# Kernel tuning notes

Hardware: AMD Instinct MI355X
Metric: run time of the kernel (lower is better)

The kernel has to match this reference:

```python
import jax, jax.numpy as jnp
import numpy as np

N = 100000   # total nodes (batched graphs)
E = 800000   # random edges (self-loops appended -> E+N total)
G = 2000     # number of graphs in batch
H = 4        # heads per GAT layer
D = 64       # hidden_size (per-head out dim)
IN = 64      # in_feats
EXTRA = 8    # extra graph-level feats
HID = H * D  # 256


def setup_inputs() -> dict:
    key = jax.random.key(0)
    ks = jax.random.split(key, 24)
    s = 0.5  # init std used in the torch module
    feats_node = jax.random.normal(ks[0], (N, IN), jnp.float32)
    feats_graph = jax.random.normal(ks[1], (G, EXTRA), jnp.float32)
    # edges + self loops (DGL GATConv requires no zero-in-degree nodes)
    src = jnp.concatenate([jax.random.randint(ks[2], (E,), 0, N), jnp.arange(N)])
    dst = jnp.concatenate([jax.random.randint(ks[3], (E,), 0, N), jnp.arange(N)])
    node_gid = jnp.sort(jax.random.randint(ks[4], (N,), 0, G))
    # GAT layer 1
    W1 = jax.random.normal(ks[5], (IN, HID), jnp.float32) * s
    al1 = jax.random.normal(ks[6], (H, D), jnp.float32) * s
    ar1 = jax.random.normal(ks[7], (H, D), jnp.float32) * s
    b1 = jnp.zeros((HID,), jnp.float32)
    # GAT layer 2
    W2 = jax.random.normal(ks[8], (HID, HID), jnp.float32) * s
    al2 = jax.random.normal(ks[9], (H, D), jnp.float32) * s
    ar2 = jax.random.normal(ks[10], (H, D), jnp.float32) * s
    b2 = jnp.zeros((HID,), jnp.float32)
    # WeightedAverage readout score
    Ws = jax.random.normal(ks[11], (HID, 1), jnp.float32) * s
    bs = jnp.zeros((1,), jnp.float32)
    # MLP: 264 -> 128 -> 64 -> 1 with SELU
    Wm1 = jax.random.normal(ks[12], (HID + EXTRA, 2 * D), jnp.float32) * s
    bm1 = jnp.zeros((2 * D,), jnp.float32)
    Wm2 = jax.random.normal(ks[13], (2 * D, D), jnp.float32) * s
    bm2 = jnp.zeros((D,), jnp.float32)
    Wm3 = jax.random.normal(ks[14], (D, 1), jnp.float32) * s
    bm3 = jnp.zeros((1,), jnp.float32)
    return dict(feats_node=feats_node, feats_graph=feats_graph,
                W1=W1, al1=al1, ar1=ar1, b1=b1,
                W2=W2, al2=al2, ar2=ar2, b2=b2,
                Ws=Ws, bs=bs, Wm1=Wm1, bm1=bm1, Wm2=Wm2, bm2=bm2,
                Wm3=Wm3, bm3=bm3,
                src=src, dst=dst, node_gid=node_gid)


def gat_layer(x, W, al, ar, b, src, dst):
    # DGL GATConv: fc -> per-node attn projections -> edge leaky_relu ->
    # edge softmax over incoming edges -> weighted scatter-sum -> +bias
    f = (x @ W).reshape(N, H, D)                       # [N,H,D]
    el = jnp.einsum('nhd,hd->nh', f, al)               # [N,H]
    er = jnp.einsum('nhd,hd->nh', f, ar)               # [N,H]
    e = jax.nn.leaky_relu(el[src] + er[dst], 0.2)      # [E',H]
    m = jax.ops.segment_max(e, dst, num_segments=N)    # per-dst max
    e = jnp.exp(e - m[dst])
    denom = jax.ops.segment_sum(e, dst, num_segments=N)
    alpha = e / denom[dst]                             # edge softmax [E',H]
    out = jax.ops.segment_sum(alpha[:, :, None] * f[src], dst, num_segments=N)
    return out.reshape(N, HID) + b


def reference(feats_node, feats_graph, W1, al1, ar1, b1, W2, al2, ar2, b2,
              Ws, bs, Wm1, bm1, Wm2, bm2, Wm3, bm3, src, dst, node_gid):
    x = jax.nn.relu(gat_layer(feats_node, W1, al1, ar1, b1, src, dst))
    x = jax.nn.relu(gat_layer(x, W2, al2, ar2, b2, src, dst))
    # weighted-average readout per graph: sum(w*x)/sum(w)
    w = jax.nn.sigmoid(x @ Ws + bs)                    # [N,1]
    num = jax.ops.segment_sum(w * x, node_gid, num_segments=G)
    den = jax.ops.segment_sum(w, node_gid, num_segments=G)
    emb = num / jnp.where(den == 0, 1.0, den)          # [G,HID]
    h = jnp.concatenate([emb, feats_graph], axis=1)    # [G,HID+EXTRA]
    h = jax.nn.selu(h @ Wm1 + bm1)
    h = jax.nn.selu(h @ Wm2 + bm2)
    return h @ Wm3 + bm3                               # [G,1]
```

## Files before the change

### kernel.cpp

```cpp
#include <hip/hip_runtime.h>
#include <hip/hip_bf16.h>
#include <math.h>

#define NN     100000
#define GG     2000
#define HH     4
#define DD     64
#define HID    256
#define INF_   64
#define EXTRA  8

typedef unsigned short u16;
typedef __attribute__((ext_vector_type(8))) short bf16x8;
typedef __attribute__((ext_vector_type(4))) float f32x4;

__device__ __forceinline__ u16 f2bf(float f) {
    unsigned u = __float_as_uint(f);
    return (u16)((u + 0x7fffu + ((u >> 16) & 1u)) >> 16);
}
__device__ __forceinline__ float bf2f(u16 v) {
    return __uint_as_float(((unsigned)v) << 16);
}

__global__ __launch_bounds__(256) void wsplit_kernel(
    const float* __restrict__ W, u16* __restrict__ hi, u16* __restrict__ lo,
    int K, int lgK)
{
    int idx = blockIdx.x * 256 + threadIdx.x;
    if (idx >= 256 * K) return;
    int n = idx >> lgK, k = idx & (K - 1);
    float w = W[k * HID + n];
    u16 h = f2bf(w);
    hi[idx] = h;
    lo[idx] = f2bf(w - bf2f(h));
}

__global__ __launch_bounds__(256) void walprep_kernel(
    const float* __restrict__ W1, const float* __restrict__ al,
    const float* __restrict__ ar, float* __restrict__ wal, float* __restrict__ war)
{
    int tid = threadIdx.x;
    int d = tid >> 2, h = tid & 3;
    const float* wrow = W1 + d * HID + h * DD;
    const float* av = al + h * DD;
    const float* bv = ar + h * DD;
    float s1 = 0.f, s2 = 0.f;
    for (int c = 0; c < DD; ++c) { s1 += wrow[c] * av[c]; s2 += wrow[c] * bv[c]; }
    wal[d * 4 + h] = s1;
    war[d * 4 + h] = s2;
}

__global__ __launch_bounds__(256) void elr1_kernel(
    const float* __restrict__ feats, const float* __restrict__ wal,
    const float* __restrict__ war, float* __restrict__ el, float* __restrict__ er)
{
    int idx = blockIdx.x * 256 + threadIdx.x;
    if (idx >= NN * HH) return;
    int n = idx >> 2, h = idx & 3;
    const float* f = feats + (size_t)n * INF_;
    float s1 = 0.f, s2 = 0.f;
    #pragma unroll 4
    for (int d = 0; d < INF_; d += 4) {
        float4 fv = *reinterpret_cast<const float4*>(f + d);
        s1 += fv.x * wal[(d + 0) * 4 + h] + fv.y * wal[(d + 1) * 4 + h]
            + fv.z * wal[(d + 2) * 4 + h] + fv.w * wal[(d + 3) * 4 + h];
        s2 += fv.x * war[(d + 0) * 4 + h] + fv.y * war[(d + 1) * 4 + h]
            + fv.z * war[(d + 2) * 4 + h] + fv.w * war[(d + 3) * 4 + h];
    }
    el[idx] = s1;
    er[idx] = s2;
}

__global__ __launch_bounds__(256) void aggregate_feats_kernel(
    const float* __restrict__ feats, const float* __restrict__ w,
    const float* __restrict__ invden, const int* __restrict__ rowptr,
    const int* __restrict__ colsrc, float* __restrict__ Y1)
{
    int t = blockIdx.x * 4 + (threadIdx.x >> 6);
    int lane = threadIdx.x & 63;
    if (t >= NN) return;
    int beg = rowptr[t], end = rowptr[t + 1];
    float a0 = 0.f, a1 = 0.f, a2 = 0.f, a3 = 0.f;
    float b0 = 0.f, b1 = 0.f, b2 = 0.f, b3 = 0.f;
    int i = beg;
    for (; i + 1 < end; i += 2) {
        int s0 = colsrc[i], s1 = colsrc[i + 1];
        float4 w0 = *reinterpret_cast<const float4*>(w + (size_t)i * 4);
        float4 w1 = *reinterpret_cast<const float4*>(w + (size_t)(i + 1) * 4);
        float f0 = feats[(size_t)s0 * INF_ + lane];
        float f1 = feats[(size_t)s1 * INF_ + lane];
        a0 += w0.x * f0; a1 += w0.y * f0; a2 += w0.z * f0; a3 += w0.w * f0;
        b0 += w1.x * f1; b1 += w1.y * f1; b2 += w1.z * f1; b3 += w1.w * f1;
    }
    if (i < end) {
        int s0 = colsrc[i];
        float4 w0 = *reinterpret_cast<const float4*>(w + (size_t)i * 4);
        float f0 = feats[(size_t)s0 * INF_ + lane];
        a0 += w0.x * f0; a1 += w0.y * f0; a2 += w0.z * f0; a3 += w0.w * f0;
    }
    float4 inv = *reinterpret_cast<const float4*>(invden + (size_t)t * 4);
    float* y = Y1 + (size_t)t * HID;
    y[lane]       = (a0 + b0) * inv.x;
    y[64 + lane]  = (a1 + b1) * inv.y;
    y[128 + lane] = (a2 + b2) * inv.z;
    y[192 + lane] = (a3 + b3) * inv.w;
}

__global__ __launch_bounds__(256) void gemm_head_kernel(
    const float* __restrict__ Y1, const u16* __restrict__ BThi,
    const u16* __restrict__ BTlo, const float* __restrict__ bias,
    float* __restrict__ X1, int M)
{
    const int tid  = threadIdx.x;
    const int wv   = tid >> 6, lane = tid & 63;
    const int quad = lane >> 4, l15 = lane & 15;
    const int r0 = blockIdx.x * 128;
    const int cbase = wv * 64;

    f32x4 acc[8][4];
    #pragma unroll
    for (int i = 0; i < 8; ++i)
        #pragma unroll
        for (int j = 0; j < 4; ++j)
            acc[i][j] = (f32x4){0.f, 0.f, 0.f, 0.f};

    #pragma unroll
    for (int k0 = 0; k0 < 64; k0 += 32) {
        bf16x8 bh[4], bl[4];
        #pragma unroll
        for (int j = 0; j < 4; ++j) {
            int n = cbase + j * 16 + l15;
            bh[j] = *reinterpret_cast<const bf16x8*>(BThi + (size_t)n * 64 + k0 + quad * 8);
            bl[j] = *reinterpret_cast<const bf16x8*>(BTlo + (size_t)n * 64 + k0 + quad * 8);
        }
        #pragma unroll
        for (int i = 0; i < 8; ++i) {
            int gr = min(r0 + i * 16 + l15, M - 1);
            const float* ap = Y1 + (size_t)gr * HID + cbase + k0 + quad * 8;
            float4 va0 = *reinterpret_cast<const float4*>(ap);
            float4 va1 = *reinterpret_cast<const float4*>(ap + 4);
            float av[8] = {va0.x, va0.y, va0.z, va0.w, va1.x, va1.y, va1.z, va1.w};
            bf16x8 vh, vl;
            #pragma unroll
            for (int m = 0; m < 8; ++m) {
                u16 h = f2bf(av[m]);
                vh[m] = (short)h;
                vl[m] = (short)f2bf(av[m] - bf2f(h));
            }
            #pragma unroll
            for (int j = 0; j < 4; ++j) {
                acc[i][j] = __builtin_amdgcn_mfma_f32_16x16x32_bf16(vh, bh[j], acc[i][j], 0, 0, 0);
                acc[i][j] = __builtin_amdgcn_mfma_f32_16x16x32_bf16(vl, bh[j], acc[i][j], 0, 0, 0);
                acc[i][j] = __builtin_amdgcn_mfma_f32_16x16x32_bf16(vh, bl[j], acc[i][j], 0, 0, 0);
            }
        }
    }
    float bv[4];
    #pragma unroll
    for (int j = 0; j < 4; ++j) bv[j] = bias[cbase + j * 16 + l15];
    #pragma unroll
    for (int i = 0; i < 8; ++i)
        #pragma unroll
        for (int rr = 0; rr < 4; ++rr) {
            int grow = r0 + i * 16 + quad * 4 + rr;
            if (grow < M) {
                float* xrow = X1 + (size_t)grow * HID + cbase + l15;
                #pragma unroll
                for (int j = 0; j < 4; ++j)
                    xrow[j * 16] = fmaxf(acc[i][j][rr] + bv[j], 0.f);
            }
        }
}

template<bool BF16_OUT>
__global__ __launch_bounds__(256) void mfma_gemm_kernel(
    const float* __restrict__ A, const u16* __restrict__ BThi,
    const u16* __restrict__ BTlo, float* __restrict__ Cf, u16* __restrict__ Cb,
    const float* __restrict__ al, const float* __restrict__ ar,
    float* __restrict__ el, float* __restrict__ er, int M, int K)
{
    __shared__ __align__(16) u16 Ah[128 * 40];
    __shared__ __align__(16) u16 Al[128 * 40];
    __shared__ __align__(16) u16 Bh[128 * 40];
    __shared__ __align__(16) u16 Bl[128 * 40];
    const int tid  = threadIdx.x;
    const int wave = tid >> 6, lane = tid & 63;
    const int quad = lane >> 4, l15 = lane & 15;
    const int wy = wave >> 1, wx = wave & 1;
    const int r0 = blockIdx.x * 128, c0 = blockIdx.y * 128;
    const int sr = tid >> 2, sseg = tid & 3;

    f32x4 acc[4][4];
    #pragma unroll
    for (int i = 0; i < 4; ++i)
        #pragma unroll
        for (int j = 0; j < 4; ++j)
            acc[i][j] = (f32x4){0.f, 0.f, 0.f, 0.f};

    for (int k0 = 0; k0 < K; k0 += 32) {
        #pragma unroll
        for (int half = 0; half < 2; ++half) {
            int r = sr + half * 64;
            int gr = min(r0 + r, M - 1);
            const float* ap = A + (size_t)gr * K + k0 + sseg * 8;
            float4 va0 = *reinterpret_cast<const float4*>(ap);
            float4 va1 = *reinterpret_cast<const float4*>(ap + 4);
            float av[8] = {va0.x, va0.y, va0.z, va0.w, va1.x, va1.y, va1.z, va1.w};
            bf16x8 vh, vl;
            #pragma unroll
            for (int m = 0; m < 8; ++m) {
                u16 h = f2bf(av[m]);
                vh[m] = (short)h;
                vl[m] = (short)f2bf(av[m] - bf2f(h));
            }
            *reinterpret_cast<bf16x8*>(&Ah[r * 40 + sseg * 8]) = vh;
            *reinterpret_cast<bf16x8*>(&Al[r * 40 + sseg * 8]) = vl;
            int gc = c0 + r;
            *reinterpret_cast<bf16x8*>(&Bh[r * 40 + sseg * 8]) =
                *reinterpret_cast<const bf16x8*>(BThi + (size_t)gc * K + k0 + sseg * 8);
            *reinterpret_cast<bf16x8*>(&Bl[r * 40 + sseg * 8]) =
                *reinterpret_cast<const bf16x8*>(BTlo + (size_t)gc * K + k0 + sseg * 8);
        }
        __syncthreads();
        bf16x8 afh[4], afl[4], bfh[4], bfl[4];
        #pragma unroll
        for (int i = 0; i < 4; ++i) {
            int row = (wy * 64 + i * 16 + l15) * 40 + quad * 8;
            afh[i] = *reinterpret_cast<const bf16x8*>(&Ah[row]);
            afl[i] = *reinterpret_cast<const bf16x8*>(&Al[row]);
        }
        #pragma unroll
        for (int j = 0; j < 4; ++j) {
            int row = (wx * 64 + j * 16 + l15) * 40 + quad * 8;
            bfh[j] = *reinterpret_cast<const bf16x8*>(&Bh[row]);
            bfl[j] = *reinterpret_cast<const bf16x8*>(&Bl[row]);
        }
        #pragma unroll
        for (int i = 0; i < 4; ++i)
            #pragma unroll
            for (int j = 0; j < 4; ++j) {
                acc[i][j] = __builtin_amdgcn_mfma_f32_16x16x32_bf16(afh[i], bfh[j], acc[i][j], 0, 0, 0);
                acc[i][j] = __builtin_amdgcn_mfma_f32_16x16x32_bf16(afl[i], bfh[j], acc[i][j], 0, 0, 0);
                acc[i][j] = __builtin_amdgcn_mfma_f32_16x16x32_bf16(afh[i], bfl[j], acc[i][j], 0, 0, 0);
            }
        __syncthreads();
    }

    #pragma unroll
    for (int i = 0; i < 4; ++i)
        #pragma unroll
        for (int rr = 0; rr < 4; ++rr) {
            int grow = r0 + wy * 64 + i * 16 + quad * 4 + rr;
            if (grow < M) {
                if (BF16_OUT) {
                    u16* crow = Cb + (size_t)grow * HID + c0 + wx * 64 + l15;
                    #pragma unroll
                    for (int j = 0; j < 4; ++j) crow[j * 16] = f2bf(acc[i][j][rr]);
                } else {
                    float* crow = Cf + (size_t)grow * HID + c0 + wx * 64 + l15;
                    #pragma unroll
                    for (int j = 0; j < 4; ++j) crow[j * 16] = acc[i][j][rr];
                }
            }
        }

    const int h = blockIdx.y * 2 + wx;
    float alf[4], arf[4];
    #pragma unroll
    for (int j = 0; j < 4; ++j) {
        alf[j] = al[h * DD + j * 16 + l15];
        arf[j] = ar[h * DD + j * 16 + l15];
    }
    #pragma unroll
    for (int i = 0; i < 4; ++i)
        #pragma unroll
        for (int rr = 0; rr < 4; ++rr) {
            float sl = acc[i][0][rr] * alf[0] + acc[i][1][rr] * alf[1]
                     + acc[i][2][rr] * alf[2] + acc[i][3][rr] * alf[3];
            float sr_ = acc[i][0][rr] * arf[0] + acc[i][1][rr] * arf[1]
                      + acc[i][2][rr] * arf[2] + acc[i][3][rr] * arf[3];
            #pragma unroll
            for (int off = 1; off < 16; off <<= 1) {
                sl  += __shfl_xor(sl, off, 64);
                sr_ += __shfl_xor(sr_, off, 64);
            }
            if (l15 == 0) {
                int grow = r0 + wy * 64 + i * 16 + quad * 4 + rr;
                if (grow < M) {
                    el[grow * 4 + h] = sl;
                    er[grow * 4 + h] = sr_;
                }
            }
        }
}

__device__ __forceinline__ float leaky02(float x) { return x > 0.f ? x : 0.2f * x; }

__global__ __launch_bounds__(256) void edge_softmax_kernel(
    const float* __restrict__ el, const float* __restrict__ er,
    const int* __restrict__ rowptr, const int* __restrict__ colsrc,
    float* __restrict__ w, float* __restrict__ invden)
{
    int idx = blockIdx.x * 256 + threadIdx.x;
    if (idx >= NN * HH) return;
    int t = idx >> 2, h = idx & 3;
    int beg = rowptr[t], end = rowptr[t + 1];
    float ert = er[idx];
    float m = -1e30f;
    for (int i = beg; i < end; ++i) {
        int s = colsrc[i];
        m = fmaxf(m, leaky02(el[s * 4 + h] + ert));
    }
    float den = 0.f;
    for (int i = beg; i < end; ++i) {
        int s = colsrc[i];
        float v = expf(leaky02(el[s * 4 + h] + ert) - m);
        w[(size_t)i * 4 + h] = v;
        den += v;
    }
    invden[idx] = 1.f / den;
}

__global__ __launch_bounds__(256) void aggregate_bf16_kernel(
    const u16* __restrict__ F, const float* __restrict__ w,
    const float* __restrict__ invden, const int* __restrict__ rowptr,
    const int* __restrict__ colsrc, const float* __restrict__ bias,
    u16* __restrict__ out)
{
    int t = blockIdx.x * 4 + (threadIdx.x >> 6);
    int lane = threadIdx.x & 63;
    if (t >= NN) return;
    int beg = rowptr[t], end = rowptr[t + 1];
    const int h = lane >> 4;
    float4 acc0 = make_float4(0.f, 0.f, 0.f, 0.f);
    float4 acc1 = make_float4(0.f, 0.f, 0.f, 0.f);
    int i = beg;
    for (; i + 1 < end; i += 2) {
        int s0 = colsrc[i], s1 = colsrc[i + 1];
        float w0 = w[(size_t)i * 4 + h];
        float w1 = w[(size_t)(i + 1) * 4 + h];
        ushort4 f0 = *reinterpret_cast<const ushort4*>(F + (size_t)s0 * HID + 4 * lane);
        ushort4 f1 = *reinterpret_cast<const ushort4*>(F + (size_t)s1 * HID + 4 * lane);
        acc0.x += w0 * bf2f(f0.x); acc0.y += w0 * bf2f(f0.y);
        acc0.z += w0 * bf2f(f0.z); acc0.w += w0 * bf2f(f0.w);
        acc1.x += w1 * bf2f(f1.x); acc1.y += w1 * bf2f(f1.y);
        acc1.z += w1 * bf2f(f1.z); acc1.w += w1 * bf2f(f1.w);
    }
    if (i < end) {
        int s0 = colsrc[i];
        float w0 = w[(size_t)i * 4 + h];
        ushort4 f0 = *reinterpret_cast<const ushort4*>(F + (size_t)s0 * HID + 4 * lane);
        acc0.x += w0 * bf2f(f0.x); acc0.y += w0 * bf2f(f0.y);
        acc0.z += w0 * bf2f(f0.z); acc0.w += w0 * bf2f(f0.w);
    }
    float inv = invden[t * 4 + h];
    float4 bv = *reinterpret_cast<const float4*>(bias + 4 * lane);
    ushort4 r;
    r.x = f2bf(fmaxf((acc0.x + acc1.x) * inv + bv.x, 0.f));
    r.y = f2bf(fmaxf((acc0.y + acc1.y) * inv + bv.y, 0.f));
    r.z = f2bf(fmaxf((acc0.z + acc1.z) * inv + bv.z, 0.f));
    r.w = f2bf(fmaxf((acc0.w + acc1.w) * inv + bv.w, 0.f));
    *reinterpret_cast<ushort4*>(out + (size_t)t * HID + 4 * lane) = r;
}

__global__ __launch_bounds__(256) void readout_kernel(
    const u16* __restrict__ X, const float* __restrict__ Ws,
    const float* __restrict__ bs, const int* __restrict__ gptr,
    float* __restrict__ emb)
{
    int g = blockIdx.x * 4 + (threadIdx.x >> 6);
    int lane = threadIdx.x & 63;
    if (g >= GG) return;
    int beg = gptr[g], end = gptr[g + 1];
    float4 wv = *reinterpret_cast<const float4*>(Ws + 4 * lane);
    float b = bs[0];
    float4 acc = make_float4(0.f, 0.f, 0.f, 0.f);
    float wsum = 0.f;
    for (int n = beg; n < end; ++n) {
        ushort4 xv = *reinterpret_cast<const ushort4*>(X + (size_t)n * HID + 4 * lane);
        float x0 = bf2f(xv.x), x1 = bf2f(xv.y), x2 = bf2f(xv.z), x3 = bf2f(xv.w);
        float p = x0 * wv.x + x1 * wv.y + x2 * wv.z + x3 * wv.w;
        #pragma unroll
        for (int off = 32; off; off >>= 1) p += __shfl_xor(p, off, 64);
        float w = 1.f / (1.f + expf(-(p + b)));
        wsum += w;
        acc.x += w * x0; acc.y += w * x1; acc.z += w * x2; acc.w += w * x3;
    }
    float inv = (wsum == 0.f) ? 1.f : wsum;
    float4 e;
    e.x = acc.x / inv; e.y = acc.y / inv; e.z = acc.z / inv; e.w = acc.w / inv;
    *reinterpret_cast<float4*>(emb + (size_t)g * HID + 4 * lane) = e;
}

__device__ __forceinline__ float selu_f(float x)
{
    const float scale = 1.0507009873554805f, alpha = 1.6732632423543772f;
    return scale * (x > 0.f ? x : alpha * expm1f(x));
}

__global__ __launch_bounds__(128) void mlp_kernel(
    const float* __restrict__ emb, const float* __restrict__ fg,
    const float* __restrict__ Wm1, const float* __restrict__ bm1,
    const float* __restrict__ Wm2, const float* __restrict__ bm2,
    const float* __restrict__ Wm3, const float* __restrict__ bm3,
    float* __restrict__ out)
{
    int g = blockIdx.x;
    __shared__ float h[HID + EXTRA];
    __shared__ float h1[128];
    __shared__ float h2[64];
    int tid = threadIdx.x;
    h[tid] = emb[(size_t)g * HID + tid];
    h[128 + tid] = emb[(size_t)g * HID + 128 + tid];
    if (tid < EXTRA) h[HID + tid] = fg[(size_t)g * EXTRA + tid];
    __syncthreads();
    float acc = bm1[tid];
    for (int i = 0; i < HID + EXTRA; ++i) acc += h[i] * Wm1[i * 128 + tid];
    h1[tid] = selu_f(acc);
    __syncthreads();
    if (tid < 64) {
        float acc2 = bm2[tid];
        for (int i = 0; i < 128; ++i) acc2 += h1[i] * Wm2[i * 64 + tid];
        h2[tid] = selu_f(acc2);
    }
    __syncthreads();
    if (tid < 64) {
        float p = h2[tid] * Wm3[tid];
        #pragma unroll
        for (int off = 32; off; off >>= 1) p += __shfl_xor(p, off, 64);
        if (tid == 0) out[g] = p + bm3[0];
    }
}

__global__ void count_dst_kernel(const int* __restrict__ dst, int* __restrict__ cnt, int E)
{
    int e = blockIdx.x * 256 + threadIdx.x;
    if (e < E) atomicAdd(&cnt[dst[e]], 1);
}
__global__ void count_gid_kernel(const int* __restrict__ gid, int* __restrict__ cnt, int n)
{
    int i = blockIdx.x * 256 + threadIdx.x;
    if (i < n) atomicAdd(&cnt[gid[i]], 1);
}
__global__ void fill_csr_kernel(const int* __restrict__ src, const int* __restrict__ dst,
                                int* __restrict__ cursor, int* __restrict__ colsrc, int E)
{
    int e = blockIdx.x * 256 + threadIdx.x;
    if (e < E) {
        int p = atomicAdd(&cursor[dst[e]], 1);
        colsrc[p] = src[e];
    }
}

__global__ __launch_bounds__(256) void scan_blocks_kernel(
    const int* __restrict__ in, int n, int* __restrict__ out, int* __restrict__ partials)
{
    __shared__ int lds[256];
    int tid = threadIdx.x;
    int base = blockIdx.x * 1024 + tid * 4;
    int v0 = (base + 0 < n) ? in[base + 0] : 0;
    int v1 = (base + 1 < n) ? in[base + 1] : 0;
    int v2 = (base + 2 < n) ? in[base + 2] : 0;
    int v3 = (base + 3 < n) ? in[base + 3] : 0;
    int s = v0 + v1 + v2 + v3;
    lds[tid] = s;
    __syncthreads();
    for (int off = 1; off < 256; off <<= 1) {
        int t = (tid >= off) ? lds[tid - off] : 0;
        __syncthreads();
        lds[tid] += t;
        __syncthreads();
    }
    int excl = lds[tid] - s;
    if (base + 0 < n) out[base + 0] = excl;
    if (base + 1 < n) out[base + 1] = excl + v0;
    if (base + 2 < n) out[base + 2] = excl + v0 + v1;
    if (base + 3 < n) out[base + 3] = excl + v0 + v1 + v2;
    if (tid == 255) partials[blockIdx.x] = lds[255];
}

__global__ __launch_bounds__(256) void scan_partials_kernel(int* partials, int nb)
{
    __shared__ int lds[256];
    int tid = threadIdx.x;
    int v = (tid < nb) ? partials[tid] : 0;
    lds[tid] = v;
    __syncthreads();
    for (int off = 1; off < 256; off <<= 1) {
        int t = (tid >= off) ? lds[tid - off] : 0;
        __syncthreads();
        lds[tid] += t;
        __syncthreads();
    }
    int excl = lds[tid] - v;
    if (tid < nb) partials[tid] = excl;
}

__global__ void add_offsets_kernel(int* __restrict__ out, const int* __restrict__ partials, int n)
{
    int i = blockIdx.x * 256 + threadIdx.x;
    if (i < n) out[i] += partials[i >> 10];
}

extern "C" void kernel_launch(void* const* d_in, const int* in_sizes, int n_in,
                              void* d_out, int out_size, void* d_ws, size_t ws_size,
                              hipStream_t stream)
{
    const float* feats_node  = (const float*)d_in[0];
    const float* feats_graph = (const float*)d_in[1];
    const float* W1  = (const float*)d_in[2];
    const float* al1 = (const float*)d_in[3];
    const float* ar1 = (const float*)d_in[4];
    const float* b1  = (const float*)d_in[5];
    const float* W2  = (const float*)d_in[6];
    const float* al2 = (const float*)d_in[7];
    const float* ar2 = (const float*)d_in[8];
    const float* b2  = (const float*)d_in[9];
    const float* Ws  = (const float*)d_in[10];
    const float* bs  = (const float*)d_in[11];
    const float* Wm1 = (const float*)d_in[12];
    const float* bm1 = (const float*)d_in[13];
    const float* Wm2 = (const float*)d_in[14];
    const float* bm2 = (const float*)d_in[15];
    const float* Wm3 = (const float*)d_in[16];
    const float* bm3 = (const float*)d_in[17];
    const int* src = (const int*)d_in[18];
    const int* dst = (const int*)d_in[19];
    const int* gid = (const int*)d_in[20];
    float* out = (float*)d_out;
    const int E = in_sizes[18];

    char* p = (char*)d_ws;
    auto alloc = [&](size_t bytes) {
        char* r = p;
        p += (bytes + 255) & ~(size_t)255;
        return r;
    };
    float* Y1     = (float*)alloc((size_t)NN * HID * 4);
    float* X      = (float*)alloc((size_t)NN * HID * 4);
    float* el     = (float*)alloc((size_t)NN * HH * 4);
    float* er     = (float*)alloc((size_t)NN * HH * 4);
    float* wbuf   = (float*)alloc((size_t)E * HH * 4);
    float* invden = (float*)alloc((size_t)NN * HH * 4);
    int*   cnt    = (int*)alloc((size_t)(NN + 1) * 4);
    int*   rowptr = (int*)alloc((size_t)(NN + 1) * 4);
    int*   colsrc = (int*)alloc((size_t)E * 4);
    int*   gcnt   = (int*)alloc((size_t)(GG + 1) * 4);
    int*   gptr   = (int*)alloc((size_t)(GG + 1) * 4);
    int*   parts  = (int*)alloc(1024 * 4);
    float* emb    = (float*)alloc((size_t)GG * HID * 4);
    u16*   BT1h   = (u16*)alloc((size_t)HID * INF_ * 2);
    u16*   BT1l   = (u16*)alloc((size_t)HID * INF_ * 2);
    u16*   BT2h   = (u16*)alloc((size_t)HID * HID * 2);
    u16*   BT2l   = (u16*)alloc((size_t)HID * HID * 2);
    float* wal1   = (float*)alloc(INF_ * HH * 4);
    float* war1   = (float*)alloc(INF_ * HH * 4);
    u16*   Fbf2   = (u16*)Y1;
    u16*   Xbf2   = (u16*)X;

    hipMemsetAsync(cnt, 0, (size_t)(NN + 1) * 4, stream);
    count_dst_kernel<<<(E + 255) / 256, 256, 0, stream>>>(dst, cnt, E);
    {
        int n = NN + 1, nb = (n + 1023) / 1024;
        scan_blocks_kernel<<<nb, 256, 0, stream>>>(cnt, n, rowptr, parts);
        scan_partials_kernel<<<1, 256, 0, stream>>>(parts, nb);
        add_offsets_kernel<<<(n + 255) / 256, 256, 0, stream>>>(rowptr, parts, n);
    }
    hipMemcpyAsync(cnt, rowptr, (size_t)(NN + 1) * 4, hipMemcpyDeviceToDevice, stream);
    fill_csr_kernel<<<(E + 255) / 256, 256, 0, stream>>>(src, dst, cnt, colsrc, E);

    hipMemsetAsync(gcnt, 0, (size_t)(GG + 1) * 4, stream);
    count_gid_kernel<<<(NN + 255) / 256, 256, 0, stream>>>(gid, gcnt, NN);
    {
        int n = GG + 1, nb = (n + 1023) / 1024;
        scan_blocks_kernel<<<nb, 256, 0, stream>>>(gcnt, n, gptr, parts);
        scan_partials_kernel<<<1, 256, 0, stream>>>(parts, nb);
        add_offsets_kernel<<<(n + 255) / 256, 256, 0, stream>>>(gptr, parts, n);
    }

    wsplit_kernel<<<(HID * INF_ + 255) / 256, 256, 0, stream>>>(W1, BT1h, BT1l, INF_, 6);
    wsplit_kernel<<<(HID * HID + 255) / 256, 256, 0, stream>>>(W2, BT2h, BT2l, HID, 8);
    walprep_kernel<<<1, 256, 0, stream>>>(W1, al1, ar1, wal1, war1);

    const int nh_blocks = (NN * HH + 255) / 256;

    elr1_kernel<<<nh_blocks, 256, 0, stream>>>(feats_node, wal1, war1, el, er);
    edge_softmax_kernel<<<nh_blocks, 256, 0, stream>>>(el, er, rowptr, colsrc, wbuf, invden);
    aggregate_feats_kernel<<<(NN + 3) / 4, 256, 0, stream>>>(feats_node, wbuf, invden,
                                                             rowptr, colsrc, Y1);
    gemm_head_kernel<<<(NN + 127) / 128, 256, 0, stream>>>(Y1, BT1h, BT1l, b1, X, NN);

    dim3 ggrid((NN + 127) / 128, HID / 128);
    mfma_gemm_kernel<true><<<ggrid, 256, 0, stream>>>(
        X, BT2h, BT2l, nullptr, Fbf2, al2, ar2, el, er, NN, HID);
    edge_softmax_kernel<<<nh_blocks, 256, 0, stream>>>(el, er, rowptr, colsrc, wbuf, invden);
    aggregate_bf16_kernel<<<(NN + 3) / 4, 256, 0, stream>>>(Fbf2, wbuf, invden, rowptr, colsrc,
                                                            b2, Xbf2);

    readout_kernel<<<(GG + 3) / 4, 256, 0, stream>>>(Xbf2, Ws, bs, gptr, emb);
    mlp_kernel<<<GG, 128, 0, stream>>>(emb, feats_graph, Wm1, bm1, Wm2, bm2, Wm3, bm3, out);
}
```

Before: 645.4 us.

## Load GEMM fragments directly from global memory and cache edge logits in softmax

The MFMA GEMM kernel no longer stages A and B tiles through shared memory with two block barriers per k-step. Each wave now loads its own A rows (splitting them into bf16 hi/lo parts) and its B fragments straight from global memory into registers. Separately, the edge softmax first pass stores the leaky-relu logits into w, so the second pass reads them back instead of re-gathering el through colsrc. The GEMM change removes LDS traffic and barriers, but the A split is now computed twice per block across the wx waves and B is read without shared reuse, which may raise global/L2 traffic.

```diff
diff --git a/kernel.cpp b/kernel.cpp
--- a/kernel.cpp
+++ b/kernel.cpp
@@ -179,16 +179,12 @@
     const float* __restrict__ al, const float* __restrict__ ar,
     float* __restrict__ el, float* __restrict__ er, int M, int K)
 {
-    __shared__ __align__(16) u16 Ah[128 * 40];
-    __shared__ __align__(16) u16 Al[128 * 40];
-    __shared__ __align__(16) u16 Bh[128 * 40];
-    __shared__ __align__(16) u16 Bl[128 * 40];
     const int tid  = threadIdx.x;
     const int wave = tid >> 6, lane = tid & 63;
     const int quad = lane >> 4, l15 = lane & 15;
     const int wy = wave >> 1, wx = wave & 1;
-    const int r0 = blockIdx.x * 128, c0 = blockIdx.y * 128;
-    const int sr = tid >> 2, sseg = tid & 3;
+    const int r0 = blockIdx.x * 128 + wy * 64;
+    const int c0 = blockIdx.y * 128 + wx * 64;
 
     f32x4 acc[4][4];
     #pragma unroll
@@ -198,11 +194,17 @@
             acc[i][j] = (f32x4){0.f, 0.f, 0.f, 0.f};
 
     for (int k0 = 0; k0 < K; k0 += 32) {
-        #pragma unroll
-        for (int half = 0; half < 2; ++half) {
-            int r = sr + half * 64;
-            int gr = min(r0 + r, M - 1);
-            const float* ap = A + (size_t)gr * K + k0 + sseg * 8;
+        bf16x8 bh[4], bl[4];
+        #pragma unroll
+        for (int j = 0; j < 4; ++j) {
+            size_t boff = (size_t)(c0 + j * 16 + l15) * K + k0 + quad * 8;
+            bh[j] = *reinterpret_cast<const bf16x8*>(BThi + boff);
+            bl[j] = *reinterpret_cast<const bf16x8*>(BTlo + boff);
+        }
+        #pragma unroll
+        for (int i = 0; i < 4; ++i) {
+            int gr = min(r0 + i * 16 + l15, M - 1);
+            const float* ap = A + (size_t)gr * K + k0 + quad * 8;
             float4 va0 = *reinterpret_cast<const float4*>(ap);
             float4 va1 = *reinterpret_cast<const float4*>(ap + 4);
             float av[8] = {va0.x, va0.y, va0.z, va0.w, va1.x, va1.y, va1.z, va1.w};
@@ -213,51 +215,27 @@
                 vh[m] = (short)h;
                 vl[m] = (short)f2bf(av[m] - bf2f(h));
             }
-            *reinterpret_cast<bf16x8*>(&Ah[r * 40 + sseg * 8]) = vh;
-            *reinterpret_cast<bf16x8*>(&Al[r * 40 + sseg * 8]) = vl;
-            int gc = c0 + r;
-            *reinterpret_cast<bf16x8*>(&Bh[r * 40 + sseg * 8]) =
-                *reinterpret_cast<const bf16x8*>(BThi + (size_t)gc * K + k0 + sseg * 8);
-            *reinterpret_cast<bf16x8*>(&Bl[r * 40 + sseg * 8]) =
-                *reinterpret_cast<const bf16x8*>(BTlo + (size_t)gc * K + k0 + sseg * 8);
-        }
-        __syncthreads();
-        bf16x8 afh[4], afl[4], bfh[4], bfl[4];
-        #pragma unroll
-        for (int i = 0; i < 4; ++i) {
-            int row = (wy * 64 + i * 16 + l15) * 40 + quad * 8;
-            afh[i] = *reinterpret_cast<const bf16x8*>(&Ah[row]);
-            afl[i] = *reinterpret_cast<const bf16x8*>(&Al[row]);
-        }
-        #pragma unroll
-        for (int j = 0; j < 4; ++j) {
-            int row = (wx * 64 + j * 16 + l15) * 40 + quad * 8;
-            bfh[j] = *reinterpret_cast<const bf16x8*>(&Bh[row]);
-            bfl[j] = *reinterpret_cast<const bf16x8*>(&Bl[row]);
-        }
-        #pragma unroll
-        for (int i = 0; i < 4; ++i)
             #pragma unroll
             for (int j = 0; j < 4; ++j) {
-                acc[i][j] = __builtin_amdgcn_mfma_f32_16x16x32_bf16(afh[i], bfh[j], acc[i][j], 0, 0, 0);
-                acc[i][j] = __builtin_amdgcn_mfma_f32_16x16x32_bf16(afl[i], bfh[j], acc[i][j], 0, 0, 0);
-                acc[i][j] = __builtin_amdgcn_mfma_f32_16x16x32_bf16(afh[i], bfl[j], acc[i][j], 0, 0, 0);
-            }
-        __syncthreads();
+                acc[i][j] = __builtin_amdgcn_mfma_f32_16x16x32_bf16(vh, bh[j], acc[i][j], 0, 0, 0);
+                acc[i][j] = __builtin_amdgcn_mfma_f32_16x16x32_bf16(vl, bh[j], acc[i][j], 0, 0, 0);
+                acc[i][j] = __builtin_amdgcn_mfma_f32_16x16x32_bf16(vh, bl[j], acc[i][j], 0, 0, 0);
+            }
+        }
     }
 
     #pragma unroll
     for (int i = 0; i < 4; ++i)
         #pragma unroll
         for (int rr = 0; rr < 4; ++rr) {
-            int grow = r0 + wy * 64 + i * 16 + quad * 4 + rr;
+            int grow = r0 + i * 16 + quad * 4 + rr;
             if (grow < M) {
                 if (BF16_OUT) {
-                    u16* crow = Cb + (size_t)grow * HID + c0 + wx * 64 + l15;
+                    u16* crow = Cb + (size_t)grow * HID + c0 + l15;
                     #pragma unroll
                     for (int j = 0; j < 4; ++j) crow[j * 16] = f2bf(acc[i][j][rr]);
                 } else {
-                    float* crow = Cf + (size_t)grow * HID + c0 + wx * 64 + l15;
+                    float* crow = Cf + (size_t)grow * HID + c0 + l15;
                     #pragma unroll
                     for (int j = 0; j < 4; ++j) crow[j * 16] = acc[i][j][rr];
                 }
@@ -285,7 +263,7 @@
                 sr_ += __shfl_xor(sr_, off, 64);
             }
             if (l15 == 0) {
-                int grow = r0 + wy * 64 + i * 16 + quad * 4 + rr;
+                int grow = r0 + i * 16 + quad * 4 + rr;
                 if (grow < M) {
                     el[grow * 4 + h] = sl;
                     er[grow * 4 + h] = sr_;
@@ -309,12 +287,13 @@
     float m = -1e30f;
     for (int i = beg; i < end; ++i) {
         int s = colsrc[i];
-        m = fmaxf(m, leaky02(el[s * 4 + h] + ert));
+        float v = leaky02(el[s * 4 + h] + ert);
+        w[(size_t)i * 4 + h] = v;
+        m = fmaxf(m, v);
     }
     float den = 0.f;
     for (int i = beg; i < end; ++i) {
-        int s = colsrc[i];
-        float v = expf(leaky02(el[s * 4 + h] + ert) - m);
+        float v = expf(w[(size_t)i * 4 + h] - m);
         w[(size_t)i * 4 + h] = v;
         den += v;
     }
```

After: 701.1 us. 1.09x slower.
